# Performance work log

Hardware: AMD Instinct MI355X
Metric: run time of the kernel (lower is better)

The kernel has to match this reference:

```python
import jax, jax.numpy as jnp
import numpy as np

N, E, DIN, DOUT = 30000, 480000, 512, 512


def setup_inputs() -> dict:
    key = jax.random.key(0)
    ks = jax.random.split(key, 20)
    inp = {}
    inp["x"] = jax.random.normal(ks[0], (N, DIN), jnp.float32)
    inp["edge_index"] = jax.random.randint(ks[1], (2, E), 0, N, dtype=jnp.int64)
    inp["edge_weight"] = jax.random.uniform(ks[2], (E,), jnp.float32)
    sc = 1.0 / np.sqrt(DIN)
    sl = 1.0 / np.sqrt(2 * DOUT)
    for i, g in enumerate(["i", "f", "g", "o"]):
        inp[f"Wc_{g}"] = jax.random.normal(ks[3 + 4 * i], (DIN, DOUT), jnp.float32) * sc
        inp[f"bc_{g}"] = jnp.zeros((DOUT,), jnp.float32)
        inp[f"Wl_{g}"] = jax.random.normal(ks[4 + 4 * i], (2 * DOUT, DOUT), jnp.float32) * sl
        inp[f"bl_{g}"] = jnp.zeros((DOUT,), jnp.float32)
    return inp


def _gcn_norm(src, dst, w, n):
    # add self loops with weight 1.0 (improved=False), then symmetric normalization
    loops = jnp.arange(n, dtype=src.dtype)
    src = jnp.concatenate([src, loops])
    dst = jnp.concatenate([dst, loops])
    w = jnp.concatenate([w, jnp.ones((n,), w.dtype)])
    deg = jax.ops.segment_sum(w, dst, num_segments=n)
    dinv = jnp.where(deg > 0, jax.lax.rsqrt(jnp.where(deg > 0, deg, 1.0)), 0.0)
    norm = dinv[src] * w * dinv[dst]
    return src, dst, norm


def reference(x, edge_index, edge_weight,
              Wc_i, bc_i, Wl_i, bl_i,
              Wc_f, bc_f, Wl_f, bl_f,
              Wc_g, bc_g, Wl_g, bl_g,
              Wc_o, bc_o, Wl_o, bl_o):
    n = x.shape[0]
    src, dst, norm = _gcn_norm(edge_index[0], edge_index[1], edge_weight, n)
    H = jnp.zeros((n, DOUT), x.dtype)  # _set_hidden_state default
    C = jnp.zeros((n, DOUT), x.dtype)  # _set_cell_state default

    def conv(Wc, bc):
        xw = x @ Wc                                        # [N, DOUT] dense GEMM
        agg = jax.ops.segment_sum(norm[:, None] * xw[src], dst, num_segments=n)
        return agg + bc

    def gate(Wc, bc, Wl, bl, act):
        z = jnp.concatenate([conv(Wc, bc), H], axis=1)      # [N, 2*DOUT]
        return act(z @ Wl + bl)

    I = gate(Wc_i, bc_i, Wl_i, bl_i, jax.nn.sigmoid)
    F = gate(Wc_f, bc_f, Wl_f, bl_f, jax.nn.sigmoid)
    G = gate(Wc_g, bc_g, Wl_g, bl_g, jnp.tanh)
    O = gate(Wc_o, bc_o, Wl_o, bl_o, jax.nn.sigmoid)
    Cn = F * C + I * G
    Hn = O * jnp.tanh(Cn)
    return O, Hn, Cn
```

## Files before the change

kernel.cpp:

```cpp
#include <hip/hip_runtime.h>
#include <stdint.h>

typedef __bf16 bf16;
typedef __attribute__((ext_vector_type(4))) float f4;
typedef __attribute__((ext_vector_type(4))) float f32x4;
typedef __attribute__((ext_vector_type(8))) __bf16 bf8v;
typedef __attribute__((ext_vector_type(4))) __bf16 bf4v;

#define NN 30000
#define MPAD 30080
#define OUTSTRIDE 15360000
#define XB 7500
#define SC_B 1875
#define TWO32 4294967296.0
#define ZN16 22504

typedef __attribute__((address_space(3))) unsigned int as3_u32;
typedef __attribute__((address_space(1))) unsigned int as1_u32;

__device__ __forceinline__ void gl_lds16(const void* g, void* l) {
  __builtin_amdgcn_global_load_lds((as1_u32*)g, (as3_u32*)l, 16, 0, 0);
}

__global__ void k_zero(f4* __restrict__ p) {
  int i = blockIdx.x * 256 + threadIdx.x;
  if (i < ZN16) { f4 z = {0.f, 0.f, 0.f, 0.f}; p[i] = z; }
}

__global__ void k_xp(const float* __restrict__ x, bf16* __restrict__ xbf,
                     const int* __restrict__ ei, const float* __restrict__ ew,
                     double* __restrict__ degcnt, int E) {
  int b = blockIdx.x;
  if (b < XB) {
    int i = b * 256 + threadIdx.x;
    const f4* x4 = (const f4*)x;
    f4 a = x4[2 * i], c = x4[2 * i + 1];
    bf8v o;
#pragma unroll
    for (int j = 0; j < 4; ++j) { o[j] = (bf16)a[j]; o[4 + j] = (bf16)c[j]; }
    ((bf8v*)xbf)[i] = o;
  } else {
    int e = (b - XB) * 256 + threadIdx.x;
    if (e < E) {
      int d = ei[E + e];
      atomicAdd(&degcnt[d], (double)ew[e] + TWO32);
    }
  }
}

__global__ void k_doffs(const double* __restrict__ degcnt, float* __restrict__ dinv,
                        int* __restrict__ gctr, int2* __restrict__ off2, int n) {
  int i = blockIdx.x * 256 + threadIdx.x;
  if (i >= n) return;
  double v = degcnt[i];
  double c = (double)(long long)(v * (1.0 / TWO32));
  int cnt = (int)c;
  float deg = (float)(v - c * TWO32);
  dinv[i] = rsqrtf(deg + 1.0f);
  int start = atomicAdd(gctr, cnt);
  off2[i] = make_int2(start, start + cnt);
}

__global__ void k_fused(const int* __restrict__ ei, const float* __restrict__ ew,
                        const float* __restrict__ dinv, const int2* __restrict__ off2,
                        int* __restrict__ cursor, int2* __restrict__ sn, int E,
                        const float* __restrict__ WcA, const float* __restrict__ WlA,
                        const float* __restrict__ WcB, const float* __restrict__ WlB,
                        const float* __restrict__ WcC, const float* __restrict__ WlC,
                        bf16* __restrict__ Wt,
                        const float* __restrict__ bcA, const float* __restrict__ blA,
                        const float* __restrict__ bcB, const float* __restrict__ blB,
                        const float* __restrict__ bcC, const float* __restrict__ blC,
                        float* __restrict__ bcomb) {
  __shared__ float sWc[32][17];
  __shared__ float sWl[16][64];
  __shared__ float smr[4][64];
  int b = blockIdx.x;
  if (b < SC_B) {
    int e = b * 256 + threadIdx.x;
    if (e >= E) return;
    int s = ei[e], d = ei[E + e];
    int pos = off2[d].x + atomicAdd(&cursor[d], 1);
    sn[pos] = make_int2(s, __float_as_int(dinv[s] * ew[e] * dinv[d]));
  } else if (b < SC_B + 384) {
    int bb = b - SC_B;
    int g = bb >> 7, rem = bb & 127;
    const float* Wc; const float* Wl;
    if (g == 0)      { Wc = WcA; Wl = WlA; }
    else if (g == 1) { Wc = WcB; Wl = WlB; }
    else             { Wc = WcC; Wl = WlC; }
    int k0 = (rem & 15) * 32, j0 = (rem >> 4) * 64;
    int t = threadIdx.x;
    int tx = t & 7, ty = t >> 3;
    float acc[2][4] = {};
    for (int c0 = 0; c0 < 512; c0 += 16) {
      if (t < 128) {
        int kk = t >> 2, c4 = (t & 3) * 4;
        f4 v = *(const f4*)(Wc + (size_t)(k0 + kk) * 512 + c0 + c4);
#pragma unroll
        for (int j = 0; j < 4; ++j) sWc[kk][c4 + j] = v[j];
      }
      { int cc = t >> 4, j4 = (t & 15) * 4;
        f4 v = *(const f4*)(Wl + (size_t)(c0 + cc) * 512 + j0 + j4);
        *(f4*)&sWl[cc][j4] = v; }
      __syncthreads();
#pragma unroll
      for (int cc = 0; cc < 16; ++cc) {
        float wcv[4], wlv[2];
#pragma unroll
        for (int q = 0; q < 4; ++q) wcv[q] = sWc[tx * 4 + q][cc];
#pragma unroll
        for (int a = 0; a < 2; ++a) wlv[a] = sWl[cc][ty * 2 + a];
#pragma unroll
        for (int a = 0; a < 2; ++a)
#pragma unroll
          for (int q = 0; q < 4; ++q) acc[a][q] += wlv[a] * wcv[q];
      }
      __syncthreads();
    }
#pragma unroll
    for (int a = 0; a < 2; ++a) {
      bf4v o;
#pragma unroll
      for (int q = 0; q < 4; ++q) o[q] = (bf16)acc[a][q];
      *(bf4v*)&Wt[((size_t)g * 512 + j0 + ty * 2 + a) * 512 + k0 + tx * 4] = o;
    }
  } else {
    int bb = b - SC_B - 384;
    int g = bb >> 3, jc = bb & 7;
    const float* bc; const float* bl; const float* Wl;
    if (g == 0)      { bc = bcA; bl = blA; Wl = WlA; }
    else if (g == 1) { bc = bcB; bl = blB; Wl = WlB; }
    else             { bc = bcC; bl = blC; Wl = WlC; }
    int jl = threadIdx.x & 63, part = threadIdx.x >> 6;
    int j = jc * 64 + jl;
    float s = 0.f;
    for (int c = part * 128; c < part * 128 + 128; ++c)
      s += bc[c] * Wl[(size_t)c * 512 + j];
    smr[part][jl] = s;
    __syncthreads();
    if (part == 0)
      bcomb[g * 512 + j] = bl[j] + smr[0][jl] + smr[1][jl] + smr[2][jl] + smr[3][jl];
  }
}

__global__ __launch_bounds__(256) void k_agg(const int2* __restrict__ off2, const int2* __restrict__ sn,
                                             const float* __restrict__ dinv, const bf16* __restrict__ xbf,
                                             bf16* __restrict__ ybf) {
  int wv = (blockIdx.x * 256 + threadIdx.x) >> 6;
  int lane = threadIdx.x & 63;
  if (wv >= MPAD) return;
  bf16* yrow = ybf + ((size_t)wv << 9) + lane * 8;
  if (wv >= NN) {
    bf8v z;
#pragma unroll
    for (int j = 0; j < 8; ++j) z[j] = (bf16)0.f;
    *(bf8v*)yrow = z;
    return;
  }
  float acc[8];
  float s0 = dinv[wv]; s0 *= s0;
  bf8v xv0 = *(const bf8v*)(xbf + ((size_t)wv << 9) + lane * 8);
#pragma unroll
  for (int j = 0; j < 8; ++j) acc[j] = s0 * (float)xv0[j];
  int2 seg = off2[wv];
  int e = seg.x, end = seg.y;
  int2 p0, p1, p2, p3;
  const bool have = (e + 4 <= end);
  if (have) { p0 = sn[e]; p1 = sn[e + 1]; p2 = sn[e + 2]; p3 = sn[e + 3]; }
  for (; e + 8 <= end; e += 4) {
    int2 q0 = sn[e + 4], q1 = sn[e + 5], q2 = sn[e + 6], q3 = sn[e + 7];
    bf8v v0 = *(const bf8v*)(xbf + ((size_t)p0.x << 9) + lane * 8);
    bf8v v1 = *(const bf8v*)(xbf + ((size_t)p1.x << 9) + lane * 8);
    bf8v v2 = *(const bf8v*)(xbf + ((size_t)p2.x << 9) + lane * 8);
    bf8v v3 = *(const bf8v*)(xbf + ((size_t)p3.x << 9) + lane * 8);
    float n0 = __int_as_float(p0.y), n1 = __int_as_float(p1.y);
    float n2 = __int_as_float(p2.y), n3 = __int_as_float(p3.y);
#pragma unroll
    for (int j = 0; j < 8; ++j)
      acc[j] += n0 * (float)v0[j] + n1 * (float)v1[j] + n2 * (float)v2[j] + n3 * (float)v3[j];
    p0 = q0; p1 = q1; p2 = q2; p3 = q3;
  }
  if (have) {
    bf8v v0 = *(const bf8v*)(xbf + ((size_t)p0.x << 9) + lane * 8);
    bf8v v1 = *(const bf8v*)(xbf + ((size_t)p1.x << 9) + lane * 8);
    bf8v v2 = *(const bf8v*)(xbf + ((size_t)p2.x << 9) + lane * 8);
    bf8v v3 = *(const bf8v*)(xbf + ((size_t)p3.x << 9) + lane * 8);
    float n0 = __int_as_float(p0.y), n1 = __int_as_float(p1.y);
    float n2 = __int_as_float(p2.y), n3 = __int_as_float(p3.y);
#pragma unroll
    for (int j = 0; j < 8; ++j)
      acc[j] += n0 * (float)v0[j] + n1 * (float)v1[j] + n2 * (float)v2[j] + n3 * (float)v3[j];
    e += 4;
  }
  for (; e < end; ++e) {
    int2 p = sn[e];
    bf8v v = *(const bf8v*)(xbf + ((size_t)p.x << 9) + lane * 8);
    float nn = __int_as_float(p.y);
#pragma unroll
    for (int j = 0; j < 8; ++j) acc[j] += nn * (float)v[j];
  }
  bf8v o;
#pragma unroll
  for (int j = 0; j < 8; ++j) o[j] = (bf16)acc[j];
  *(bf8v*)yrow = o;
}

__global__ __launch_bounds__(256, 5) void k_gemm(const bf16* __restrict__ A, const bf16* __restrict__ Bt,
                                                 const float* __restrict__ bcomb, float* __restrict__ out) {
  __shared__ __align__(16) char lds[32768];
  const int t = threadIdx.x, lane = t & 63, w = t >> 6;
  const int wm = w >> 1, wn = w & 1;
  const int d = blockIdx.x;
  const int s = (d & 7) * 470 + (d >> 3);
  const int m0 = (s >> 3) * 64, n0 = (s & 7) * 64;
  const int l15 = lane & 15, lhi = lane >> 4;
  f32x4 acc[3][2][2] = {};

  const int lq = lane >> 2;
  const int sw = (lane >> 3) & 3;
  const int kcol = 16 * ((lane & 3) ^ sw);
  const int rswz = 16 * (lhi ^ ((l15 >> 1) & 3));

  const char* aS = (const char*)A + ((size_t)(m0 + w * 16 + lq) << 10) + kcol;
  const char* bS[3];
#pragma unroll
  for (int i = 0; i < 3; ++i) {
    int bi = i * 4 + w, g = bi >> 2, q = bi & 3;
    bS[i] = (const char*)Bt + ((size_t)(g * 512 + n0 + q * 16 + lq) << 10) + kcol;
  }
  const int vA = (wm * 32 + l15) * 64 + rswz;
  const int vB = 4096 + (wn * 32 + l15) * 64 + rswz;

  auto stage = [&](int bufoff, int kp) {
    gl_lds16(aS + kp * 64, lds + bufoff + w * 1024 + lane * 16);
#pragma unroll
    for (int i = 0; i < 3; ++i)
      gl_lds16(bS[i] + kp * 64, lds + bufoff + 4096 + (i * 4 + w) * 1024 + lane * 16);
  };

  auto compute = [&](int bufoff) {
    bf8v af[2];
#pragma unroll
    for (int mi = 0; mi < 2; ++mi)
      af[mi] = *(const bf8v*)(lds + bufoff + vA + mi * 1024);
#pragma unroll
    for (int g = 0; g < 3; ++g) {
      bf8v b0 = *(const bf8v*)(lds + bufoff + vB + g * 4096);
      bf8v b1 = *(const bf8v*)(lds + bufoff + vB + g * 4096 + 1024);
#pragma unroll
      for (int mi = 0; mi < 2; ++mi) {
        acc[g][mi][0] = __builtin_amdgcn_mfma_f32_16x16x32_bf16(b0, af[mi], acc[g][mi][0], 0, 0, 0);
        acc[g][mi][1] = __builtin_amdgcn_mfma_f32_16x16x32_bf16(b1, af[mi], acc[g][mi][1], 0, 0, 0);
      }
    }
  };

  stage(0, 0);
  stage(16384, 1);
#pragma unroll
  for (int kp = 0; kp < 16; ++kp) {
    if (kp < 15) asm volatile("s_waitcnt vmcnt(4)" ::: "memory");
    else         asm volatile("s_waitcnt vmcnt(0)" ::: "memory");
    __builtin_amdgcn_sched_barrier(0);
    __builtin_amdgcn_s_barrier();
    __builtin_amdgcn_sched_barrier(0);
    compute((kp & 1) * 16384);
    __builtin_amdgcn_sched_barrier(0);
    __builtin_amdgcn_s_barrier();
    __builtin_amdgcn_sched_barrier(0);
    if (kp < 14) stage((kp & 1) * 16384, kp + 2);
  }

#pragma unroll
  for (int ni = 0; ni < 2; ++ni) {
    int nb = n0 + wn * 32 + ni * 16 + lhi * 4;
    f4 bI = *(const f4*)&bcomb[nb];
    f4 bG = *(const f4*)&bcomb[512 + nb];
    f4 bO = *(const f4*)&bcomb[1024 + nb];
#pragma unroll
    for (int mi = 0; mi < 2; ++mi) {
      int row = m0 + wm * 32 + mi * 16 + l15;
      if (row < NN) {
        f4 vO, vH, vC;
#pragma unroll
        for (int r = 0; r < 4; ++r) {
          float zi = acc[0][mi][ni][r] + bI[r];
          float zg = acc[1][mi][ni][r] + bG[r];
          float zo = acc[2][mi][ni][r] + bO[r];
          float I = 1.f / (1.f + __expf(-zi));
          float e2g = __expf(2.f * zg);
          float G = (e2g - 1.f) / (e2g + 1.f);
          float O = 1.f / (1.f + __expf(-zo));
          float Cn = I * G;
          float e2c = __expf(2.f * Cn);
          float tc = (e2c - 1.f) / (e2c + 1.f);
          vO[r] = O; vH[r] = O * tc; vC[r] = Cn;
        }
        size_t base = ((size_t)row << 9) + nb;
        __builtin_nontemporal_store(vO, (f4*)&out[base]);
        __builtin_nontemporal_store(vH, (f4*)&out[OUTSTRIDE + base]);
        __builtin_nontemporal_store(vC, (f4*)&out[2 * OUTSTRIDE + base]);
      }
    }
  }
}

extern "C" void kernel_launch(void* const* d_in, const int* in_sizes, int n_in,
                              void* d_out, int out_size, void* d_ws, size_t ws_size,
                              hipStream_t stream) {
  const float* x   = (const float*)d_in[0];
  const int*   ei  = (const int*)d_in[1];
  const float* ew  = (const float*)d_in[2];
  const float* Wc_i = (const float*)d_in[3];
  const float* bc_i = (const float*)d_in[4];
  const float* Wl_i = (const float*)d_in[5];
  const float* bl_i = (const float*)d_in[6];
  const float* Wc_g = (const float*)d_in[11];
  const float* bc_g = (const float*)d_in[12];
  const float* Wl_g = (const float*)d_in[13];
  const float* bl_g = (const float*)d_in[14];
  const float* Wc_o = (const float*)d_in[15];
  const float* bc_o = (const float*)d_in[16];
  const float* Wl_o = (const float*)d_in[17];
  const float* bl_o = (const float*)d_in[18];

  const int E = in_sizes[2];
  const int n = in_sizes[0] / 512;
  const int NB = (n + 255) / 256;

  char* ws = (char*)d_ws;
  bf16*  ybf   = (bf16*)ws;
  float* dinv  = (float*)(ws + 30801920);
  bf16*  Wt    = (bf16*)(ws + 30924800);
  float* bcomb = (float*)(ws + 32497664);
  (void)ws_size;

  char* ob = (char*)d_out;
  float*  out    = (float*)d_out;
  bf16*   xbf    = (bf16*)ob;
  int2*   sn     = (int2*)(ob + 30720000);
  double* degcnt = (double*)(ob + 34560000);
  int*    curs   = (int*)(ob + 34800000);
  int*    gctr   = (int*)(ob + 34920000);
  int2*   off2   = (int2*)(ob + 34920064);
  (void)out_size; (void)n_in;

  k_zero<<<(ZN16 + 255) / 256, 256, 0, stream>>>((f4*)degcnt);
  k_xp<<<XB + (E + 255) / 256, 256, 0, stream>>>(x, xbf, ei, ew, degcnt, E);
  k_doffs<<<NB, 256, 0, stream>>>(degcnt, dinv, gctr, off2, n);
  k_fused<<<SC_B + 384 + 24, 256, 0, stream>>>(ei, ew, dinv, off2, curs, sn, E,
                                               Wc_i, Wl_i, Wc_g, Wl_g, Wc_o, Wl_o, Wt,
                                               bc_i, bl_i, bc_g, bl_g, bc_o, bl_o, bcomb);
  k_agg<<<(MPAD * 64 + 255) / 256, 256, 0, stream>>>(off2, sn, dinv, xbf, ybf);
  k_gemm<<<3760, 256, 0, stream>>>(ybf, Wt, bcomb, out);
}
```

Measured before the change: 273.6 us.

## Seed cursors with segment starts, deepen gather pipeline, use nontemporal loads/stores

The offsets kernel now writes each node's segment start into its cursor array, so the scatter kernel no longer reads off2 and the cursor region no longer needs zeroing, which shrinks the zero kernel. The aggregation kernel gathers 8 neighbour rows per iteration instead of 4, with the next 8 edge records prefetched, and reads the packed edge records as 64-bit nontemporal loads. Output rows are written with nontemporal stores. The deeper unroll raises memory-level parallelism in the gather, at the cost of more registers and a longer scalar tail for nodes with fewer than 8 edges.

```diff
diff --git a/kernel.cpp b/kernel.cpp
--- a/kernel.cpp
+++ b/kernel.cpp
@@ -13,7 +13,7 @@
 #define XB 7500
 #define SC_B 1875
 #define TWO32 4294967296.0
-#define ZN16 22504
+#define ZN16 15004
 
 typedef __attribute__((address_space(3))) unsigned int as3_u32;
 typedef __attribute__((address_space(1))) unsigned int as1_u32;
@@ -49,7 +49,8 @@
 }
 
 __global__ void k_doffs(const double* __restrict__ degcnt, float* __restrict__ dinv,
-                        int* __restrict__ gctr, int2* __restrict__ off2, int n) {
+                        int* __restrict__ gctr, int* __restrict__ curs,
+                        int2* __restrict__ off2, int n) {
   int i = blockIdx.x * 256 + threadIdx.x;
   if (i >= n) return;
   double v = degcnt[i];
@@ -58,11 +59,12 @@
   float deg = (float)(v - c * TWO32);
   dinv[i] = rsqrtf(deg + 1.0f);
   int start = atomicAdd(gctr, cnt);
+  curs[i] = start;
   off2[i] = make_int2(start, start + cnt);
 }
 
 __global__ void k_fused(const int* __restrict__ ei, const float* __restrict__ ew,
-                        const float* __restrict__ dinv, const int2* __restrict__ off2,
+                        const float* __restrict__ dinv,
                         int* __restrict__ cursor, int2* __restrict__ sn, int E,
                         const float* __restrict__ WcA, const float* __restrict__ WlA,
                         const float* __restrict__ WcB, const float* __restrict__ WlB,
@@ -80,7 +82,7 @@
     int e = b * 256 + threadIdx.x;
     if (e >= E) return;
     int s = ei[e], d = ei[E + e];
-    int pos = off2[d].x + atomicAdd(&cursor[d], 1);
+    int pos = atomicAdd(&cursor[d], 1);
     sn[pos] = make_int2(s, __float_as_int(dinv[s] * ew[e] * dinv[d]));
   } else if (b < SC_B + 384) {
     int bb = b - SC_B;
@@ -144,7 +146,7 @@
   }
 }
 
-__global__ __launch_bounds__(256) void k_agg(const int2* __restrict__ off2, const int2* __restrict__ sn,
+__global__ __launch_bounds__(256) void k_agg(const int2* __restrict__ off2, const long long* __restrict__ sn,
                                              const float* __restrict__ dinv, const bf16* __restrict__ xbf,
                                              bf16* __restrict__ ybf) {
   int wv = (blockIdx.x * 256 + threadIdx.x) >> 6;
@@ -155,7 +157,7 @@
     bf8v z;
 #pragma unroll
     for (int j = 0; j < 8; ++j) z[j] = (bf16)0.f;
-    *(bf8v*)yrow = z;
+    __builtin_nontemporal_store(z, (bf8v*)yrow);
     return;
   }
   float acc[8];
@@ -165,45 +167,45 @@
   for (int j = 0; j < 8; ++j) acc[j] = s0 * (float)xv0[j];
   int2 seg = off2[wv];
   int e = seg.x, end = seg.y;
-  int2 p0, p1, p2, p3;
-  const bool have = (e + 4 <= end);
-  if (have) { p0 = sn[e]; p1 = sn[e + 1]; p2 = sn[e + 2]; p3 = sn[e + 3]; }
-  for (; e + 8 <= end; e += 4) {
-    int2 q0 = sn[e + 4], q1 = sn[e + 5], q2 = sn[e + 6], q3 = sn[e + 7];
-    bf8v v0 = *(const bf8v*)(xbf + ((size_t)p0.x << 9) + lane * 8);
-    bf8v v1 = *(const bf8v*)(xbf + ((size_t)p1.x << 9) + lane * 8);
-    bf8v v2 = *(const bf8v*)(xbf + ((size_t)p2.x << 9) + lane * 8);
-    bf8v v3 = *(const bf8v*)(xbf + ((size_t)p3.x << 9) + lane * 8);
-    float n0 = __int_as_float(p0.y), n1 = __int_as_float(p1.y);
-    float n2 = __int_as_float(p2.y), n3 = __int_as_float(p3.y);
+  long long m[8];
+  bool have8 = (e + 8 <= end);
+  if (have8) {
+#pragma unroll
+    for (int j = 0; j < 8; ++j) m[j] = __builtin_nontemporal_load(sn + e + j);
+  }
+  while (have8) {
+    long long mn[8];
+    bool next = (e + 16 <= end);
+    if (next) {
+#pragma unroll
+      for (int j = 0; j < 8; ++j) mn[j] = __builtin_nontemporal_load(sn + e + 8 + j);
+    }
+    bf8v v[8];
 #pragma unroll
     for (int j = 0; j < 8; ++j)
-      acc[j] += n0 * (float)v0[j] + n1 * (float)v1[j] + n2 * (float)v2[j] + n3 * (float)v3[j];
-    p0 = q0; p1 = q1; p2 = q2; p3 = q3;
-  }
-  if (have) {
-    bf8v v0 = *(const bf8v*)(xbf + ((size_t)p0.x << 9) + lane * 8);
-    bf8v v1 = *(const bf8v*)(xbf + ((size_t)p1.x << 9) + lane * 8);
-    bf8v v2 = *(const bf8v*)(xbf + ((size_t)p2.x << 9) + lane * 8);
-    bf8v v3 = *(const bf8v*)(xbf + ((size_t)p3.x << 9) + lane * 8);
-    float n0 = __int_as_float(p0.y), n1 = __int_as_float(p1.y);
-    float n2 = __int_as_float(p2.y), n3 = __int_as_float(p3.y);
-#pragma unroll
-    for (int j = 0; j < 8; ++j)
-      acc[j] += n0 * (float)v0[j] + n1 * (float)v1[j] + n2 * (float)v2[j] + n3 * (float)v3[j];
-    e += 4;
+      v[j] = *(const bf8v*)(xbf + ((size_t)(int)(m[j] & 0xFFFFFFFFll) << 9) + lane * 8);
+#pragma unroll
+    for (int j = 0; j < 8; ++j) {
+      float nrm = __int_as_float((int)(m[j] >> 32));
+#pragma unroll
+      for (int q = 0; q < 8; ++q) acc[q] += nrm * (float)v[j][q];
+    }
+    e += 8;
+#pragma unroll
+    for (int j = 0; j < 8; ++j) m[j] = mn[j];
+    have8 = next;
   }
   for (; e < end; ++e) {
-    int2 p = sn[e];
-    bf8v v = *(const bf8v*)(xbf + ((size_t)p.x << 9) + lane * 8);
-    float nn = __int_as_float(p.y);
-#pragma unroll
-    for (int j = 0; j < 8; ++j) acc[j] += nn * (float)v[j];
+    long long p = __builtin_nontemporal_load(sn + e);
+    bf8v v = *(const bf8v*)(xbf + ((size_t)(int)(p & 0xFFFFFFFFll) << 9) + lane * 8);
+    float nn = __int_as_float((int)(p >> 32));
+#pragma unroll
+    for (int q = 0; q < 8; ++q) acc[q] += nn * (float)v[q];
   }
   bf8v o;
 #pragma unroll
   for (int j = 0; j < 8; ++j) o[j] = (bf16)acc[j];
-  *(bf8v*)yrow = o;
+  __builtin_nontemporal_store(o, (bf8v*)yrow);
 }
 
 __global__ __launch_bounds__(256, 5) void k_gemm(const bf16* __restrict__ A, const bf16* __restrict__ Bt,
@@ -341,17 +343,17 @@
   bf16*   xbf    = (bf16*)ob;
   int2*   sn     = (int2*)(ob + 30720000);
   double* degcnt = (double*)(ob + 34560000);
-  int*    curs   = (int*)(ob + 34800000);
-  int*    gctr   = (int*)(ob + 34920000);
+  int*    gctr   = (int*)(ob + 34800000);
+  int*    curs   = (int*)(ob + 34800064);
   int2*   off2   = (int2*)(ob + 34920064);
   (void)out_size; (void)n_in;
 
   k_zero<<<(ZN16 + 255) / 256, 256, 0, stream>>>((f4*)degcnt);
   k_xp<<<XB + (E + 255) / 256, 256, 0, stream>>>(x, xbf, ei, ew, degcnt, E);
-  k_doffs<<<NB, 256, 0, stream>>>(degcnt, dinv, gctr, off2, n);
-  k_fused<<<SC_B + 384 + 24, 256, 0, stream>>>(ei, ew, dinv, off2, curs, sn, E,
+  k_doffs<<<NB, 256, 0, stream>>>(degcnt, dinv, gctr, curs, off2, n);
+  k_fused<<<SC_B + 384 + 24, 256, 0, stream>>>(ei, ew, dinv, curs, sn, E,
                                                Wc_i, Wl_i, Wc_g, Wl_g, Wc_o, Wl_o, Wt,
                                                bc_i, bl_i, bc_g, bl_g, bc_o, bl_o, bcomb);
-  k_agg<<<(MPAD * 64 + 255) / 256, 256, 0, stream>>>(off2, sn, dinv, xbf, ybf);
+  k_agg<<<(MPAD * 64 + 255) / 256, 256, 0, stream>>>(off2, (const long long*)sn, dinv, xbf, ybf);
   k_gemm<<<3760, 256, 0, stream>>>(ybf, Wt, bcomb, out);
 }
```

Result: slower. 298.9 us (+9.2%).
